# Optimization experiments

Hardware: AMD Instinct MI355X
Metric: run time of the kernel (lower is better)

## Reference

```python
import jax, jax.numpy as jnp
import numpy as np

B, T, HID = 2, 2048, 1024
H, D = 16, 64
ROPE = 32
GIDX = (2, 3, 4, 5)
MASK_VAL = -1e9


def setup_inputs() -> dict:
    key = jax.random.key(0)
    ks = jax.random.split(key, 5)
    x = jax.random.normal(ks[0], (B, T, HID), jnp.float32)
    mask = jnp.triu(jnp.ones((T, T), jnp.bool_), 1)  # True above diagonal -> masked (causal)
    qkv_w = jax.random.normal(ks[1], (3 * H * D, HID), jnp.float32) * (1.0 / np.sqrt(HID))
    qkv_b = jax.random.normal(ks[2], (3 * H * D,), jnp.float32) * 0.02
    out_w = jax.random.normal(ks[3], (HID, H * D), jnp.float32) * (1.0 / np.sqrt(H * D))
    out_b = jax.random.normal(ks[4], (HID,), jnp.float32) * 0.02
    return {"x": x, "mask": mask, "qkv_w": qkv_w, "qkv_b": qkv_b, "out_w": out_w, "out_b": out_b}


def _rope_tables(t):
    inv_freq = 1.0 / (10000.0 ** (jnp.arange(0, ROPE, 2, dtype=jnp.float32) / ROPE))
    freqs = jnp.arange(t, dtype=jnp.float32)[:, None] * inv_freq[None, :]  # [T, ROPE/2]
    return jnp.cos(freqs), jnp.sin(freqs)


def _apply_rotary(x, cos, sin):
    # x: [B,H,T,D]; rotate first ROPE dims as interleaved pairs
    xr = x[..., :ROPE].reshape(*x.shape[:-1], ROPE // 2, 2)
    x1, x2 = xr[..., 0], xr[..., 1]
    rot = jnp.stack([x1 * cos - x2 * sin, x1 * sin + x2 * cos], axis=-1).reshape(*x.shape[:-1], ROPE)
    return jnp.concatenate([rot, x[..., ROPE:]], axis=-1)


def reference(x, mask, qkv_w, qkv_b, out_w, out_b):
    b, t, _ = x.shape
    qkv = x @ qkv_w.T + qkv_b                      # [B,T,3*H*D]
    q, k, v = jnp.split(qkv, 3, axis=-1)
    q, k, v = [y.reshape(b, t, H, D).transpose(0, 2, 1, 3) for y in (q, k, v)]  # [B,H,T,D]
    cos, sin = _rope_tables(t)                      # [T, ROPE/2] broadcast over B,H
    q = _apply_rotary(q, cos, sin)
    k = _apply_rotary(k, cos, sin)
    scale = 1.0 / np.sqrt(D)
    # local dense causal attention
    scores = jnp.einsum('bhqd,bhkd->bhqk', q, k) * scale
    scores = jnp.where(mask, MASK_VAL, scores)
    out_local = jnp.einsum('bhqk,bhkd->bhqd', jax.nn.softmax(scores, axis=-1), v)
    # global token pass with its own causal overlay
    gidx = jnp.array(GIDX)
    gq = q[:, :, gidx]                              # [B,H,G,D]
    gs = jnp.einsum('bhgd,bhkd->bhgk', gq, k) * scale
    gmask = jnp.arange(t)[None, :] > gidx[:, None]  # [G,T]: col > row -> masked
    gs = jnp.where(gmask, MASK_VAL, gs)
    gout = jnp.einsum('bhgk,bhkd->bhgd', jax.nn.softmax(gs, axis=-1), v)
    out = out_local.at[:, :, gidx].set(gout)
    attn_out = out.transpose(0, 2, 1, 3).reshape(b, t, H * D)
    return attn_out @ out_w.T + out_b
```

## Files before the change

### kernel.cpp

```cpp
#include <hip/hip_runtime.h>
#include <math.h>

typedef unsigned short u16;
typedef unsigned int u32;
typedef __attribute__((ext_vector_type(4))) float f32x4;
typedef __attribute__((ext_vector_type(16))) float f32x16;
typedef __attribute__((ext_vector_type(8))) short bf16x8;

#define B_ 2
#define T_ 2048
#define H_ 16
#define HID 1024
#define NQKV 3072
#define M_ 4096
#define SCALE_Q 0.18033688011112042f

__device__ __forceinline__ u16 f2bf(float f) {
  union { float f; unsigned u; } v; v.f = f;
  unsigned r = v.u + 0x7FFFu + ((v.u >> 16) & 1u);
  return (u16)(r >> 16);
}
__device__ __forceinline__ float bf2f(u16 u) {
  union { unsigned u; float f; } v; v.u = ((unsigned)u) << 16; return v.f;
}
__device__ __forceinline__ u32 cvt_pk_bf16(float lo, float hi) {
  u32 r;
  asm("v_cvt_pk_bf16_f32 %0, %1, %2" : "=v"(r) : "v"(lo), "v"(hi));
  return r;
}
__device__ __forceinline__ void perm32swap(u32& a, u32& b) {
  asm volatile("v_permlane32_swap_b32 %0, %1" : "+v"(a), "+v"(b));
}
__device__ __forceinline__ float fexp2(float x) { return __builtin_amdgcn_exp2f(x); }

__device__ __forceinline__ void gload16(const void* g, void* l) {
  __builtin_amdgcn_global_load_lds((const __attribute__((address_space(1))) void*)g,
                                   (__attribute__((address_space(3))) void*)l, 16, 0, 0);
}

__global__ void prep(const float* __restrict__ x, const float* __restrict__ qkv_w,
                     const float* __restrict__ out_w, u16* __restrict__ xb,
                     u16* __restrict__ wqkv, u16* __restrict__ wout, float* __restrict__ tab) {
  int bid = blockIdx.x;
  if (bid < 128) {
    int i = bid * 256 + threadIdx.x;
    int tpos = i >> 4, f = i & 15;
    float ang = (float)tpos * exp2f(-(float)f * 0.83048202372184058696f);
    float s, c;
    sincosf(ang, &s, &c);
    tab[i * 2] = c;
    tab[i * 2 + 1] = s;
    return;
  }
  bid -= 128;
  const float* in;
  u16* out;
  if (bid < 4096) { in = x; out = xb; }
  else if (bid < 7168) { bid -= 4096; in = qkv_w; out = wqkv; }
  else { bid -= 7168; in = out_w; out = wout; }
  int i = bid * 256 + threadIdx.x;
  float4 v = ((const float4*)in)[i];
  uint2 o;
  o.x = (unsigned)f2bf(v.x) | ((unsigned)f2bf(v.y) << 16);
  o.y = (unsigned)f2bf(v.z) | ((unsigned)f2bf(v.w) << 16);
  ((uint2*)out)[i] = o;
}

__global__ __launch_bounds__(256) void gemm_qkv(const u16* __restrict__ A,
    const u16* __restrict__ Bt, const float* __restrict__ bias, const float* __restrict__ tab,
    u16* __restrict__ Q, u16* __restrict__ K, u16* __restrict__ Vt)
{
  __shared__ u16 lsA[2][128 * 32];
  __shared__ u16 lsB[2][128 * 32];
  const int t = threadIdx.x;
  const int l = t & 63, w = t >> 6;
  const int wm = (w >> 1) * 64, wn = (w & 1) * 64;
  const int lr = l & 15, lg = l >> 4;
  const long bm = (long)blockIdx.y * 128, bn = (long)blockIdx.x * 128;
  const int KD = HID;

  f32x4 acc[4][4];
#pragma unroll
  for (int i = 0; i < 4; i++)
#pragma unroll
    for (int j = 0; j < 4; j++) acc[i][j] = (f32x4){0.f, 0.f, 0.f, 0.f};

  const int srow = l >> 2, sko = (l & 3) * 8;
  const u16* Ab = A + (bm + srow) * (long)KD + sko;
  const u16* Bb = Bt + (bn + srow) * (long)KD + sko;

  auto stage = [&](int buf, int k0) {
#pragma unroll
    for (int g = 0; g < 2; g++)
      gload16(Ab + (long)((w * 2 + g) * 16) * KD + k0, &lsA[buf][(w * 2 + g) * 512]);
#pragma unroll
    for (int g = 0; g < 2; g++)
      gload16(Bb + (long)((w * 2 + g) * 16) * KD + k0, &lsB[buf][(w * 2 + g) * 512]);
  };

  stage(0, 0);
  __syncthreads();
  int cur = 0;
  for (int k0 = 0; k0 < KD; k0 += 32) {
    if (k0 + 32 < KD) stage(cur ^ 1, k0 + 32);
    bf16x8 af[4], bfv[4];
#pragma unroll
    for (int mi = 0; mi < 4; mi++)
      af[mi] = *(const bf16x8*)&lsA[cur][(wm + mi * 16 + lr) * 32 + lg * 8];
#pragma unroll
    for (int ni = 0; ni < 4; ni++)
      bfv[ni] = *(const bf16x8*)&lsB[cur][(wn + ni * 16 + lr) * 32 + lg * 8];
    __builtin_amdgcn_s_setprio(1);
#pragma unroll
    for (int mi = 0; mi < 4; mi++)
#pragma unroll
      for (int ni = 0; ni < 4; ni++)
        acc[mi][ni] = __builtin_amdgcn_mfma_f32_16x16x32_bf16(af[mi], bfv[ni], acc[mi][ni], 0, 0, 0);
    __builtin_amdgcn_s_setprio(0);
    __syncthreads();
    cur ^= 1;
  }

  const int region = (int)(bn >> 10);
  const int h = (int)(((bn + wn) & 1023) >> 6);
  const float2* tab2 = (const float2*)tab;
  u16* QK = (region == 0) ? Q : K;

#pragma unroll
  for (int mi = 0; mi < 4; mi++) {
    const int m0 = (int)(bm) + wm + mi * 16 + lg * 4;
    const int b = m0 >> 11, t0 = m0 & (T_ - 1);
    const long bh = b * 16 + h;
#pragma unroll
    for (int ni = 0; ni < 4; ni++) {
      const int d = ni * 16 + lr;
      const long col = bn + wn + d;
      const float bv = bias[col];
      float vv[4];
#pragma unroll
      for (int r = 0; r < 4; r++) vv[r] = acc[mi][ni][r] + bv;
      if (region < 2 && ni < 2) {
        const int fi = d >> 1;
        const float sgn = (d & 1) ? 1.f : -1.f;
#pragma unroll
        for (int r = 0; r < 4; r++) {
          float pvv = __shfl_xor(vv[r], 1, 64);
          float2 cs = tab2[(t0 + r) * 16 + fi];
          vv[r] = vv[r] * cs.x + sgn * pvv * cs.y;
        }
      }
      if (region == 0) {
#pragma unroll
        for (int r = 0; r < 4; r++) vv[r] *= SCALE_Q;
      }
      if (region < 2) {
#pragma unroll
        for (int r = 0; r < 4; r++)
          QK[(bh * T_ + t0 + r) * 64 + d] = f2bf(vv[r]);
      } else {
        uint2 pk;
        pk.x = cvt_pk_bf16(vv[0], vv[1]);
        pk.y = cvt_pk_bf16(vv[2], vv[3]);
        *(uint2*)&Vt[(bh * 64 + d) * (long)T_ + t0] = pk;
      }
    }
  }
}

__global__ __launch_bounds__(256) void gemm_out(const u16* __restrict__ A,
    const u16* __restrict__ Bt, const float* __restrict__ bias,
    float* __restrict__ outp, int N, int K)
{
  constexpr int BM = 64;
  constexpr int MI = 4, NI = 2;
  __shared__ u16 lsA[2][BM * 32];
  __shared__ u16 lsB[2][128 * 32];
  const int t = threadIdx.x;
  const int l = t & 63, w = t >> 6;
  const int wn = w * 32;
  const int lr = l & 15, lg = l >> 4;
  const long bm = (long)blockIdx.y * BM, bn = (long)blockIdx.x * 128;

  f32x4 acc[MI][NI];
#pragma unroll
  for (int i = 0; i < MI; i++)
#pragma unroll
    for (int j = 0; j < NI; j++) acc[i][j] = (f32x4){0.f, 0.f, 0.f, 0.f};

  const int srow = l >> 2, sko = (l & 3) * 8;
  const u16* Ab = A + (bm + srow) * (long)K + sko;
  const u16* Bb = Bt + (bn + srow) * (long)K + sko;

  auto stage = [&](int buf, int k0) {
    gload16(Ab + (long)(w * 16) * K + k0, &lsA[buf][w * 512]);
    gload16(Bb + (long)(w * 16) * K + k0, &lsB[buf][w * 512]);
    gload16(Bb + (long)((w + 4) * 16) * K + k0, &lsB[buf][(w + 4) * 512]);
  };

  stage(0, 0);
  __syncthreads();
  int cur = 0;
  for (int k0 = 0; k0 < K; k0 += 32) {
    if (k0 + 32 < K) stage(cur ^ 1, k0 + 32);
    bf16x8 af[MI], bfv[NI];
#pragma unroll
    for (int mi = 0; mi < MI; mi++)
      af[mi] = *(const bf16x8*)&lsA[cur][(mi * 16 + lr) * 32 + lg * 8];
#pragma unroll
    for (int ni = 0; ni < NI; ni++)
      bfv[ni] = *(const bf16x8*)&lsB[cur][(wn + ni * 16 + lr) * 32 + lg * 8];
    __builtin_amdgcn_s_setprio(1);
#pragma unroll
    for (int mi = 0; mi < MI; mi++)
#pragma unroll
      for (int ni = 0; ni < NI; ni++)
        acc[mi][ni] = __builtin_amdgcn_mfma_f32_16x16x32_bf16(af[mi], bfv[ni], acc[mi][ni], 0, 0, 0);
    __builtin_amdgcn_s_setprio(0);
    __syncthreads();
    cur ^= 1;
  }
#pragma unroll
  for (int mi = 0; mi < MI; mi++)
#pragma unroll
    for (int ni = 0; ni < NI; ni++) {
      long row = bm + mi * 16 + lg * 4;
      long col = bn + wn + ni * 16 + lr;
      float bv = bias[col];
#pragma unroll
      for (int r = 0; r < 4; r++)
        outp[(row + r) * (long)N + col] = acc[mi][ni][r] + bv;
    }
}

__global__ __launch_bounds__(128, 2) void fattn(const u16* __restrict__ Q, const u16* __restrict__ Kp,
                                                const u16* __restrict__ V, u16* __restrict__ O) {
  const int id = blockIdx.x;
  const int qs = 31 - (id >> 5);
  const int bh = id & 31;
  __shared__ u16 lsK[2][64 * 64];
  __shared__ u16 lsV[2][64 * 64];
  const int t = threadIdx.x, l = t & 63, w = t >> 6;
  const int lq = l & 31, hi = l >> 5;
  const u16* Qb = Q + (long)bh * T_ * 64;
  const u16* Kb = Kp + (long)bh * T_ * 64;
  const u16* Vb = V + (long)bh * 64 * T_;
  const int qbase = qs * 64 + w * 32;
  const int qg = qbase + lq;

  bf16x8 aq[4];
#pragma unroll
  for (int ds = 0; ds < 4; ds++)
    aq[ds] = *(const bf16x8*)&Qb[(long)qg * 64 + ds * 16 + hi * 8];

  f32x16 oac[2];
#pragma unroll
  for (int d0 = 0; d0 < 2; d0++)
#pragma unroll
    for (int i = 0; i < 16; i++) oac[d0][i] = 0.f;
  float mrow = -1e30f, lrow = 0.f;

  const int srow = l >> 3;
  const int scx = ((l & 7) ^ srow) * 8;
  long kgo[4], vgo[4];
#pragma unroll
  for (int g = 0; g < 4; g++) {
    kgo[g] = (long)(32 * w + 8 * g + srow) * 64 + scx;
    vgo[g] = (long)(32 * w + 8 * g + srow) * T_ + scx;
  }
  auto stage = [&](int buf, const u16* kp, const u16* vp) {
#pragma unroll
    for (int g = 0; g < 4; g++) {
      gload16(kp + kgo[g], &lsK[buf][(4 * w + g) * 512]);
      gload16(vp + vgo[g], &lsV[buf][(4 * w + g) * 512]);
    }
  };

  stage(0, Kb, Vb);
  __syncthreads();

  int cur = 0;
  for (int kt = 0; kt <= qs; kt++) {
    if (kt < qs)
      stage(cur ^ 1, Kb + (long)(kt + 1) * 4096, Vb + (long)(kt + 1) * 64);

    f32x16 s2[2];
#pragma unroll
    for (int ks2 = 0; ks2 < 2; ks2++)
#pragma unroll
      for (int i = 0; i < 16; i++) s2[ks2][i] = 0.f;
    __builtin_amdgcn_s_setprio(1);
#pragma unroll
    for (int ds = 0; ds < 4; ds++)
#pragma unroll
      for (int ks2 = 0; ks2 < 2; ks2++) {
        int arow = ks2 * 32 + lq;
        bf16x8 kf = *(const bf16x8*)&lsK[cur][arow * 64 + ((ds * 16 + hi * 8) ^ ((arow & 7) * 8))];
        s2[ks2] = __builtin_amdgcn_mfma_f32_32x32x16_bf16(kf, aq[ds], s2[ks2], 0, 0, 0);
      }
    __builtin_amdgcn_s_setprio(0);

    if (kt == qs) {
      const int kbase = kt * 64;
#pragma unroll
      for (int ks2 = 0; ks2 < 2; ks2++)
#pragma unroll
        for (int rg = 0; rg < 16; rg++) {
          int kglob = kbase + ks2 * 32 + (rg & 3) + 8 * (rg >> 2) + 4 * hi;
          if (kglob > qg) s2[ks2][rg] = -1e30f;
        }
    }

    float tv[16];
#pragma unroll
    for (int i = 0; i < 16; i++) tv[i] = fmaxf(s2[0][i], s2[1][i]);
#pragma unroll
    for (int i = 0; i < 8; i++) tv[i] = fmaxf(tv[i], tv[i + 8]);
#pragma unroll
    for (int i = 0; i < 4; i++) tv[i] = fmaxf(tv[i], tv[i + 4]);
    float mx = fmaxf(fmaxf(tv[0], tv[1]), fmaxf(tv[2], tv[3]));
    mx = fmaxf(mx, __shfl_xor(mx, 32, 64));

    if (__any(mx - mrow > 8.f)) {
      float newm = fmaxf(mrow, mx);
      float sf = fexp2(mrow - newm);
      mrow = newm;
      lrow *= sf;
#pragma unroll
      for (int d0 = 0; d0 < 2; d0++)
#pragma unroll
        for (int i = 0; i < 16; i++) oac[d0][i] *= sf;
    }

    float pv[32];
#pragma unroll
    for (int ks2 = 0; ks2 < 2; ks2++)
#pragma unroll
      for (int rg = 0; rg < 16; rg++) pv[ks2 * 16 + rg] = fexp2(s2[ks2][rg] - mrow);

    float sv[16];
#pragma unroll
    for (int i = 0; i < 16; i++) sv[i] = pv[i] + pv[i + 16];
#pragma unroll
    for (int i = 0; i < 8; i++) sv[i] = sv[i] + sv[i + 8];
#pragma unroll
    for (int i = 0; i < 4; i++) sv[i] = sv[i] + sv[i + 4];
    float rs = (sv[0] + sv[1]) + (sv[2] + sv[3]);
    rs += __shfl_xor(rs, 32, 64);
    lrow += rs;

    bf16x8 pf[2][2];
#pragma unroll
    for (int ks2 = 0; ks2 < 2; ks2++)
#pragma unroll
      for (int s = 0; s < 2; s++) {
        u32 a0 = cvt_pk_bf16(pv[ks2 * 16 + 8 * s + 0], pv[ks2 * 16 + 8 * s + 1]);
        u32 b0 = cvt_pk_bf16(pv[ks2 * 16 + 8 * s + 4], pv[ks2 * 16 + 8 * s + 5]);
        u32 a1 = cvt_pk_bf16(pv[ks2 * 16 + 8 * s + 2], pv[ks2 * 16 + 8 * s + 3]);
        u32 b1 = cvt_pk_bf16(pv[ks2 * 16 + 8 * s + 6], pv[ks2 * 16 + 8 * s + 7]);
        perm32swap(a0, b0);
        perm32swap(a1, b1);
        uint4 fr = make_uint4(a0, a1, b0, b1);
        pf[ks2][s] = *(bf16x8*)&fr;
      }

    __builtin_amdgcn_s_setprio(1);
#pragma unroll
    for (int d0 = 0; d0 < 2; d0++)
#pragma unroll
      for (int ks2 = 0; ks2 < 2; ks2++)
#pragma unroll
        for (int s = 0; s < 2; s++) {
          int arow = d0 * 32 + lq;
          bf16x8 vb = *(const bf16x8*)&lsV[cur][arow * 64 +
                          ((ks2 * 32 + s * 16 + hi * 8) ^ ((arow & 7) * 8))];
          oac[d0] = __builtin_amdgcn_mfma_f32_32x32x16_bf16(vb, pf[ks2][s], oac[d0], 0, 0, 0);
        }
    __builtin_amdgcn_s_setprio(0);

    if (kt < qs) __syncthreads();
    cur ^= 1;
  }

  const int b = bh >> 4, h = bh & 15;
  const float inv = 1.f / lrow;
  u16* obase = O + ((long)(b * T_ + qg)) * 1024 + h * 64;
#pragma unroll
  for (int d0 = 0; d0 < 2; d0++)
#pragma unroll
    for (int rp = 0; rp < 8; rp++) {
      int rg = rp * 2;
      int d = d0 * 32 + (rg & 3) + 8 * (rg >> 2) + 4 * hi;
      u32 pk = cvt_pk_bf16(oac[d0][rg] * inv, oac[d0][rg + 1] * inv);
      *(u32*)&obase[d] = pk;
    }
}

extern "C" void kernel_launch(void* const* d_in, const int* in_sizes, int n_in,
                              void* d_out, int out_size, void* d_ws, size_t ws_size,
                              hipStream_t stream) {
  (void)in_sizes; (void)n_in; (void)out_size; (void)ws_size;
  const float* x     = (const float*)d_in[0];
  const float* qkv_w = (const float*)d_in[2];
  const float* qkv_b = (const float*)d_in[3];
  const float* out_w = (const float*)d_in[4];
  const float* out_b = (const float*)d_in[5];
  char* ws = (char*)d_ws;
  size_t off = 0;
  auto alloc = [&](size_t n) { void* p = ws + off; off += (n + 255) & ~(size_t)255; return p; };
  u16*   xb    = (u16*)alloc((size_t)M_ * HID * 2);
  u16*   wqkv  = (u16*)alloc((size_t)NQKV * HID * 2);
  u16*   wout  = (u16*)alloc((size_t)HID * HID * 2);
  u16*   Qb    = (u16*)alloc((size_t)M_ * HID * 2);
  u16*   Kb    = (u16*)alloc((size_t)M_ * HID * 2);
  u16*   Vtb   = (u16*)alloc((size_t)M_ * HID * 2);
  u16*   attnb = (u16*)alloc((size_t)M_ * HID * 2);
  float* tab   = (float*)alloc((size_t)T_ * 16 * 2 * 4);

  prep<<<8320, 256, 0, stream>>>(x, qkv_w, out_w, xb, wqkv, wout, tab);
  gemm_qkv<<<dim3(NQKV / 128, M_ / 128), 256, 0, stream>>>(xb, wqkv, qkv_b, tab, Qb, Kb, Vtb);
  fattn<<<1024, 128, 0, stream>>>(Qb, Kb, Vtb, attnb);
  gemm_out<<<dim3(HID / 128, M_ / 64), 256, 0, stream>>>(attnb, wout, out_b, (float*)d_out, HID, HID);
}
```

Before: 197.7 us.

## Triple-buffer LDS staging in QKV and output GEMMs with partial vmcnt waits

```diff
diff --git a/kernel.cpp b/kernel.cpp
--- a/kernel.cpp
+++ b/kernel.cpp
@@ -70,8 +70,8 @@
     const u16* __restrict__ Bt, const float* __restrict__ bias, const float* __restrict__ tab,
     u16* __restrict__ Q, u16* __restrict__ K, u16* __restrict__ Vt)
 {
-  __shared__ u16 lsA[2][128 * 32];
-  __shared__ u16 lsB[2][128 * 32];
+  __shared__ u16 lsA[3][128 * 32];
+  __shared__ u16 lsB[3][128 * 32];
   const int t = threadIdx.x;
   const int l = t & 63, w = t >> 6;
   const int wm = (w >> 1) * 64, wn = (w & 1) * 64;
@@ -99,10 +99,17 @@
   };
 
   stage(0, 0);
-  __syncthreads();
+  stage(1, 32);
+  __builtin_amdgcn_sched_barrier(0);
+  asm volatile("s_waitcnt vmcnt(4)" ::: "memory");
+  __builtin_amdgcn_s_barrier();
+  __builtin_amdgcn_sched_barrier(0);
+
   int cur = 0;
   for (int k0 = 0; k0 < KD; k0 += 32) {
-    if (k0 + 32 < KD) stage(cur ^ 1, k0 + 32);
+    int nxt = cur + 1; if (nxt == 3) nxt = 0;
+    int nx2 = nxt + 1; if (nx2 == 3) nx2 = 0;
+    if (k0 + 64 < KD) stage(nx2, k0 + 64);
     bf16x8 af[4], bfv[4];
 #pragma unroll
     for (int mi = 0; mi < 4; mi++)
@@ -117,8 +124,17 @@
       for (int ni = 0; ni < 4; ni++)
         acc[mi][ni] = __builtin_amdgcn_mfma_f32_16x16x32_bf16(af[mi], bfv[ni], acc[mi][ni], 0, 0, 0);
     __builtin_amdgcn_s_setprio(0);
-    __syncthreads();
-    cur ^= 1;
+    __builtin_amdgcn_sched_barrier(0);
+    if (k0 + 64 < KD) {
+      asm volatile("s_waitcnt vmcnt(4)" ::: "memory");
+    } else if (k0 + 32 < KD) {
+      asm volatile("s_waitcnt vmcnt(0)" ::: "memory");
+    }
+    if (k0 + 32 < KD) {
+      __builtin_amdgcn_s_barrier();
+      __builtin_amdgcn_sched_barrier(0);
+    }
+    cur = nxt;
   }
 
   const int region = (int)(bn >> 10);
@@ -173,8 +189,8 @@
 {
   constexpr int BM = 64;
   constexpr int MI = 4, NI = 2;
-  __shared__ u16 lsA[2][BM * 32];
-  __shared__ u16 lsB[2][128 * 32];
+  __shared__ u16 lsA[3][BM * 32];
+  __shared__ u16 lsB[3][128 * 32];
   const int t = threadIdx.x;
   const int l = t & 63, w = t >> 6;
   const int wn = w * 32;
@@ -198,10 +214,17 @@
   };
 
   stage(0, 0);
-  __syncthreads();
+  stage(1, 32);
+  __builtin_amdgcn_sched_barrier(0);
+  asm volatile("s_waitcnt vmcnt(3)" ::: "memory");
+  __builtin_amdgcn_s_barrier();
+  __builtin_amdgcn_sched_barrier(0);
+
   int cur = 0;
   for (int k0 = 0; k0 < K; k0 += 32) {
-    if (k0 + 32 < K) stage(cur ^ 1, k0 + 32);
+    int nxt = cur + 1; if (nxt == 3) nxt = 0;
+    int nx2 = nxt + 1; if (nx2 == 3) nx2 = 0;
+    if (k0 + 64 < K) stage(nx2, k0 + 64);
     bf16x8 af[MI], bfv[NI];
 #pragma unroll
     for (int mi = 0; mi < MI; mi++)
@@ -216,8 +239,17 @@
       for (int ni = 0; ni < NI; ni++)
         acc[mi][ni] = __builtin_amdgcn_mfma_f32_16x16x32_bf16(af[mi], bfv[ni], acc[mi][ni], 0, 0, 0);
     __builtin_amdgcn_s_setprio(0);
-    __syncthreads();
-    cur ^= 1;
+    __builtin_amdgcn_sched_barrier(0);
+    if (k0 + 64 < K) {
+      asm volatile("s_waitcnt vmcnt(3)" ::: "memory");
+    } else if (k0 + 32 < K) {
+      asm volatile("s_waitcnt vmcnt(0)" ::: "memory");
+    }
+    if (k0 + 32 < K) {
+      __builtin_amdgcn_s_barrier();
+      __builtin_amdgcn_sched_barrier(0);
+    }
+    cur = nxt;
   }
 #pragma unroll
   for (int mi = 0; mi < MI; mi++)
```

Result: slower. 238.2 us (+20.5%).
